# Performance work log

Measured on AMD Instinct MI355X. Metric: run time of the kernel, lower is better.

Reference implementation:

```python
import jax, jax.numpy as jnp
import numpy as np

B = 16
LEN_X = [1024, 896, 768, 640, 512, 1000, 750, 600, 1024, 512, 700, 800, 900, 950, 650, 550]
LEN_M = LEN_X[::-1]
MAXX, MAXM = 1024, 1024
D, H, DH, DFF = 512, 8, 64, 2048
EPS = 1e-5


def _ids(lens):
    seg = np.repeat(np.arange(len(lens)), lens).astype(np.int32)
    pos = np.concatenate([np.arange(l) for l in lens]).astype(np.int32)
    return seg, pos


def _layernorm(x, g, b):
    m = jnp.mean(x, axis=-1, keepdims=True)
    v = jnp.mean((x - m) ** 2, axis=-1, keepdims=True)  # biased var, as torch LN
    return (x - m) * jax.lax.rsqrt(v + EPS) * g + b


def setup_inputs() -> dict:
    key = jax.random.key(0)
    ks = jax.random.split(key, 8)
    TX, TM = sum(LEN_X), sum(LEN_M)
    seg_x, pos_x = _ids(LEN_X)
    seg_m, pos_m = _ids(LEN_M)

    def xavier(k, shape):  # nn.init.xavier_uniform_
        a = float(np.sqrt(6.0 / (shape[0] + shape[1])))
        return jax.random.uniform(k, shape, jnp.float32, -a, a)

    return {
        "x": jax.random.normal(ks[0], (TX, D), jnp.float32),
        "mem": jax.random.normal(ks[1], (TM, D), jnp.float32),
        "Wq": xavier(ks[2], (H * DH, D)),
        "Wk": xavier(ks[3], (H * DH, D)),
        "Wv": xavier(ks[4], (H * DH, D)),
        "Wo": xavier(ks[5], (D, H * DH)),
        "W1": xavier(ks[6], (DFF, D)),
        "b1": jnp.zeros((DFF,), jnp.float32),
        "W2": xavier(ks[7], (D, DFF)),
        "b2": jnp.zeros((D,), jnp.float32),
        "g_in": jnp.ones((D,), jnp.float32),
        "b_in": jnp.zeros((D,), jnp.float32),
        "g_inter": jnp.ones((D,), jnp.float32),
        "b_inter": jnp.zeros((D,), jnp.float32),
        "lengths_x": jnp.array(LEN_X, jnp.int32),
        "lengths_mem": jnp.array(LEN_M, jnp.int32),
        "seg_x": jnp.array(seg_x),
        "pos_x": jnp.array(pos_x),
        "seg_m": jnp.array(seg_m),
        "pos_m": jnp.array(pos_m),
    }


def reference(x, mem, Wq, Wk, Wv, Wo, W1, b1, W2, b2,
              g_in, b_in, g_inter, b_inter,
              lengths_x, lengths_mem, seg_x, pos_x, seg_m, pos_m):
    # --- self_attention(norm_in(x), mem) ---
    h = _layernorm(x, g_in, b_in)
    q = (h @ Wq.T).reshape(-1, H, DH)     # [Tx,H,DH]
    k = (mem @ Wk.T).reshape(-1, H, DH)   # [Tm,H,DH]
    v = (mem @ Wv.T).reshape(-1, H, DH)

    # pad_packed_tensor via scatter (value 0)
    qp = jnp.zeros((B, MAXX, H, DH), q.dtype).at[seg_x, pos_x].set(q)
    kp = jnp.zeros((B, MAXM, H, DH), k.dtype).at[seg_m, pos_m].set(k)
    vp = jnp.zeros((B, MAXM, H, DH), v.dtype).at[seg_m, pos_m].set(v)

    e = jnp.einsum('bxhd,byhd->bhxy', qp, kp) / np.sqrt(DH)  # [B,H,X,Y]

    xm = jnp.arange(MAXX)[None, :] < lengths_x[:, None]   # [B,X]
    ym = jnp.arange(MAXM)[None, :] < lengths_mem[:, None]  # [B,Y]
    mask = (xm[:, :, None] & ym[:, None, :])[:, None]      # [B,1,X,Y]

    e = jnp.where(mask, e, -1e9)
    alpha = jax.nn.softmax(e, axis=-1)
    alpha = jnp.where(mask, alpha, 0.0)

    out = jnp.einsum('bhxy,byhd->bxhd', alpha, vp)         # [B,X,H,DH]
    out = out.reshape(B, MAXX, H * DH) @ Wo.T              # [B,X,D]
    attn = out[seg_x, pos_x]                               # pack_padded_tensor

    x = x + attn
    # --- FFN block ---
    h2 = _layernorm(x, g_inter, b_inter)
    x = x + (jax.nn.relu(h2 @ W1.T + b1) @ W2.T + b2)
    return x
```

## Files before the change

kernel.cpp:

```cpp
#include <hip/hip_runtime.h>

#define TXT 12276
#define DM  512
#define NH  8
#define DHD 64
#define DFF 2048

typedef _Float16 half_t;
typedef _Float16 half8 __attribute__((ext_vector_type(8)));
typedef _Float16 half4v __attribute__((ext_vector_type(4)));
typedef float f32x4 __attribute__((ext_vector_type(4)));

__constant__ int c_offx[16] = {0,1024,1920,2688,3328,3840,4840,5590,6190,7214,7726,8426,9226,10126,11076,11726};
__constant__ int c_lenx[16] = {1024,896,768,640,512,1000,750,600,1024,512,700,800,900,950,650,550};
__constant__ int c_offm[16] = {0,550,1200,2150,3050,3850,4550,5062,6086,6686,7436,8436,8948,9588,10356,11252};
__constant__ int c_lenm[16] = {550,650,950,900,800,700,512,1024,600,750,1000,512,640,768,896,1024};
__constant__ int c_qtcum[17] = {0,16,30,42,52,60,76,88,98,114,122,133,146,161,176,187,196};

enum { EPI_NONE = 0, EPI_RES = 1, EPI_BIAS_RELU = 2, EPI_BIAS_RES = 3 };

__device__ __forceinline__ void gload_lds16(const void* g, void* l) {
    __builtin_amdgcn_global_load_lds((const __attribute__((address_space(1))) uint32_t*)g,
                                     (__attribute__((address_space(3))) uint32_t*)l, 16, 0, 0);
}

template<int EPI, int OUT_HALF, int PIPE>
__global__ __launch_bounds__(256)
void gemm_h(const half_t* __restrict__ A, const half_t* __restrict__ B,
            void* __restrict__ Cv, const float* __restrict__ bias,
            const float* __restrict__ res, int M, int N, int K)
{
    constexpr int NBUF = PIPE ? 2 : 1;
    __shared__ __align__(16) half_t As[NBUF*128*64];
    __shared__ __align__(16) half_t Bs[NBUF*128*64];

    const int t    = threadIdx.x;
    const int lane = t & 63;
    const int wv   = t >> 6;
    const int id   = blockIdx.x;
    const int wid  = (id & 7) * (gridDim.x >> 3) + (id >> 3);
    const int NY   = N >> 7;
    const int m0   = (wid / NY) * 128;
    const int n0   = (wid % NY) * 128;
    const int wr   = (wv >> 1) * 64;
    const int wc   = (wv & 1) * 64;
    const int fr   = lane & 15;
    const int fq   = lane >> 4;
    const int srow   = lane >> 3;
    const int schunk = (lane & 7) ^ srow;

    f32x4 acc[4][4];
    #pragma unroll
    for (int m = 0; m < 4; ++m)
        #pragma unroll
        for (int n = 0; n < 4; ++n) acc[m][n] = (f32x4){0.f,0.f,0.f,0.f};

    auto stage = [&](int k0, half_t* as, half_t* bs) {
        #pragma unroll
        for (int jj = 0; jj < 4; ++jj) {
            const int j    = wv * 4 + jj;
            const int rowt = j * 8 + srow;
            int ra = m0 + rowt; ra = (ra < M) ? ra : (M - 1);
            gload_lds16(A + (size_t)ra * K + k0 + schunk * 8, as + j * 512);
            gload_lds16(B + (size_t)(n0 + rowt) * K + k0 + schunk * 8, bs + j * 512);
        }
    };
    auto compute = [&](const half_t* as, const half_t* bs) {
        #pragma unroll
        for (int kk = 0; kk < 2; ++kk) {
            half8 af[4], bf[4];
            #pragma unroll
            for (int m = 0; m < 4; ++m) {
                const int row  = wr + m * 16 + fr;
                const int boff = (kk * 64 + fq * 16) ^ ((row & 7) << 4);
                af[m] = *(const half8*)((const char*)as + row * 128 + boff);
            }
            #pragma unroll
            for (int n = 0; n < 4; ++n) {
                const int row  = wc + n * 16 + fr;
                const int boff = (kk * 64 + fq * 16) ^ ((row & 7) << 4);
                bf[n] = *(const half8*)((const char*)bs + row * 128 + boff);
            }
            #pragma unroll
            for (int m = 0; m < 4; ++m)
                #pragma unroll
                for (int n = 0; n < 4; ++n)
                    acc[m][n] = __builtin_amdgcn_mfma_f32_16x16x32_f16(af[m], bf[n], acc[m][n], 0, 0, 0);
        }
    };

    if (PIPE == 0) {
        for (int k0 = 0; k0 < K; k0 += 64) {
            stage(k0, As, Bs);
            __syncthreads();
            compute(As, Bs);
            __syncthreads();
        }
    } else {
        stage(0, As, Bs);
        __syncthreads();
        int cur = 0;
        for (int k0 = 0; k0 < K; k0 += 64) {
            if (k0 + 64 < K)
                stage(k0 + 64, As + (cur ^ 1) * 8192, Bs + (cur ^ 1) * 8192);
            compute(As + cur * 8192, Bs + cur * 8192);
            __syncthreads();
            cur ^= 1;
        }
    }

    #pragma unroll
    for (int n = 0; n < 4; ++n) {
        const int col = n0 + wc + n * 16 + fr;
        const float bsv = (EPI == EPI_BIAS_RELU || EPI == EPI_BIAS_RES) ? bias[col] : 0.f;
        #pragma unroll
        for (int m = 0; m < 4; ++m) {
            const f32x4 a = acc[m][n];
            #pragma unroll
            for (int r = 0; r < 4; ++r) {
                const int row = m0 + wr + m * 16 + fq * 4 + r;
                if (row < M) {
                    float v = a[r];
                    if (EPI == EPI_BIAS_RELU || EPI == EPI_BIAS_RES) v += bsv;
                    if (EPI == EPI_BIAS_RELU) v = fmaxf(v, 0.f);
                    if (EPI == EPI_RES || EPI == EPI_BIAS_RES) v += res[(size_t)row * N + col];
                    if (OUT_HALF) ((half_t*)Cv)[(size_t)row * N + col] = (half_t)v;
                    else          ((float*) Cv)[(size_t)row * N + col] = v;
                }
            }
        }
    }
}

__global__ __launch_bounds__(256)
void f2h_w(const float* __restrict__ Wq, const float* __restrict__ Wk,
           const float* __restrict__ Wv, const float* __restrict__ Wo,
           const float* __restrict__ W1, const float* __restrict__ W2,
           half_t* __restrict__ HW)
{
    const int i = blockIdx.x * 256 + threadIdx.x;
    const float* src; int off;
    if      (i < 65536)  { src = Wq; off = 0;      }
    else if (i < 131072) { src = Wk; off = 65536;  }
    else if (i < 196608) { src = Wv; off = 131072; }
    else if (i < 262144) { src = Wo; off = 196608; }
    else if (i < 524288) { src = W1; off = 262144; }
    else                 { src = W2; off = 524288; }
    float4 v = ((const float4*)src)[i - off];
    half4v h = {(_Float16)v.x, (_Float16)v.y, (_Float16)v.z, (_Float16)v.w};
    ((half4v*)HW)[i] = h;
}

__global__ __launch_bounds__(256)
void f2h(const float* __restrict__ in, half_t* __restrict__ out, int n4)
{
    int i = blockIdx.x * 256 + threadIdx.x;
    if (i < n4) {
        float4 v = ((const float4*)in)[i];
        half4v h = {(_Float16)v.x, (_Float16)v.y, (_Float16)v.z, (_Float16)v.w};
        ((half4v*)out)[i] = h;
    }
}

template<int OUT_HALF>
__global__ __launch_bounds__(256)
void layernorm_k(const float* __restrict__ in, const float* __restrict__ g,
                 const float* __restrict__ b, void* __restrict__ outv, int nrows)
{
    const int wave = threadIdx.x >> 6;
    const int lane = threadIdx.x & 63;
    const int row  = blockIdx.x * 4 + wave;
    if (row >= nrows) return;
    const float* px = in + (size_t)row * DM;
    float4 v0 = *(const float4*)(px + lane*4);
    float4 v1 = *(const float4*)(px + 256 + lane*4);

    float s = v0.x+v0.y+v0.z+v0.w + v1.x+v1.y+v1.z+v1.w;
    #pragma unroll
    for (int off = 1; off < 64; off <<= 1) s += __shfl_xor(s, off);
    float mean = s * (1.f/512.f);

    float dx0 = v0.x-mean, dy0 = v0.y-mean, dz0 = v0.z-mean, dw0 = v0.w-mean;
    float dx1 = v1.x-mean, dy1 = v1.y-mean, dz1 = v1.z-mean, dw1 = v1.w-mean;
    float q = dx0*dx0+dy0*dy0+dz0*dz0+dw0*dw0 + dx1*dx1+dy1*dy1+dz1*dz1+dw1*dw1;
    #pragma unroll
    for (int off = 1; off < 64; off <<= 1) q += __shfl_xor(q, off);
    float inv = rsqrtf(q * (1.f/512.f) + 1e-5f);

    float4 g0 = *(const float4*)(g + lane*4);
    float4 g1 = *(const float4*)(g + 256 + lane*4);
    float4 b0 = *(const float4*)(b + lane*4);
    float4 b1 = *(const float4*)(b + 256 + lane*4);
    float4 o0, o1;
    o0.x = dx0*inv*g0.x + b0.x; o0.y = dy0*inv*g0.y + b0.y;
    o0.z = dz0*inv*g0.z + b0.z; o0.w = dw0*inv*g0.w + b0.w;
    o1.x = dx1*inv*g1.x + b1.x; o1.y = dy1*inv*g1.y + b1.y;
    o1.z = dz1*inv*g1.z + b1.z; o1.w = dw1*inv*g1.w + b1.w;

    if (OUT_HALF) {
        half_t* po = (half_t*)outv + (size_t)row * DM;
        half4v h0 = {(_Float16)o0.x,(_Float16)o0.y,(_Float16)o0.z,(_Float16)o0.w};
        half4v h1 = {(_Float16)o1.x,(_Float16)o1.y,(_Float16)o1.z,(_Float16)o1.w};
        *(half4v*)(po + lane*4)       = h0;
        *(half4v*)(po + 256 + lane*4) = h1;
    } else {
        float* po = (float*)outv + (size_t)row * DM;
        *(float4*)(po + lane*4)       = o0;
        *(float4*)(po + 256 + lane*4) = o1;
    }
}

__global__ __launch_bounds__(256)
void attn_k(const half_t* __restrict__ q, const half_t* __restrict__ k,
            const half_t* __restrict__ v, half_t* __restrict__ o, int ldkv)
{
    __shared__ __align__(16) half_t Qs[64*64];
    __shared__ __align__(16) half_t Ks[2][64*64];
    __shared__ __align__(16) half_t Vt[2][64*64];
    __shared__ __align__(16) half_t Ps[4*16*72];

    const int t    = threadIdx.x;
    const int lane = t & 63;
    const int w    = t >> 6;
    const int fr   = lane & 15;
    const int fq   = lane >> 4;
    const int id   = blockIdx.x;
    const int hh   = id & 7;
    const int tile = id >> 3;
    int b = 0;
    while (tile >= c_qtcum[b+1]) ++b;
    const int qt0 = (tile - c_qtcum[b]) * 64;
    const int lx = c_lenx[b], lm = c_lenm[b];
    const int ox = c_offx[b], om = c_offm[b];
    const int qrem = lx - qt0;

    const int srow   = lane >> 3;
    const int schunk = (lane & 7) ^ srow;

    #pragma unroll
    for (int jj = 0; jj < 2; ++jj) {
        const int j   = w * 2 + jj;
        const int row = j * 8 + srow;
        const int rc  = (row < qrem) ? row : qrem - 1;
        gload_lds16(q + (size_t)(ox + qt0 + rc) * DM + hh * DHD + schunk * 8, &Qs[j * 512]);
    }

    const int nt = (lm + 63) >> 6;

    auto stageK = [&](int yt, int buf) {
        const int y0 = yt * 64, yrem = lm - y0;
        #pragma unroll
        for (int jj = 0; jj < 2; ++jj) {
            const int j   = w * 2 + jj;
            const int row = j * 8 + srow;
            const int rc  = (row < yrem) ? row : yrem - 1;
            gload_lds16(k + (size_t)(om + y0 + rc) * ldkv + hh * DHD + schunk * 8, &Ks[buf][j * 512]);
        }
    };
    auto loadV = [&](int yt, half8& va, half8& vb) {
        const int y0 = yt * 64, yrem = lm - y0;
        const int y  = lane;
        const int yc = (y < yrem) ? y : yrem - 1;
        const half_t* vp = v + (size_t)(om + y0 + yc) * ldkv + hh * DHD;
        va = *(const half8*)(vp + w * 8);
        vb = *(const half8*)(vp + (w + 4) * 8);
    };
    auto writeV = [&](int buf, half8 va, half8 vb) {
        const int y = lane;
        #pragma unroll
        for (int jd = 0; jd < 8; ++jd) {
            const int da = w * 8 + jd;
            const int db = (w + 4) * 8 + jd;
            *(half_t*)((char*)&Vt[buf][0] + da * 128 + ((2 * y) ^ ((da & 7) << 4))) = va[jd];
            *(half_t*)((char*)&Vt[buf][0] + db * 128 + ((2 * y) ^ ((db & 7) << 4))) = vb[jd];
        }
    };

    {
        stageK(0, 0);
        half8 va, vb;
        loadV(0, va, vb);
        writeV(0, va, vb);
    }
    __syncthreads();

    f32x4 accO[4];
    float m_run[4], l_run[4];
    #pragma unroll
    for (int r = 0; r < 4; ++r) {
        m_run[r] = -1e30f; l_run[r] = 0.f;
        accO[r] = (f32x4){0.f,0.f,0.f,0.f};
    }

    int buf = 0;
    for (int yt = 0; yt < nt; ++yt) {
        const int yrem = lm - yt * 64;
        const bool pf = (yt + 1 < nt);
        half8 va, vb;
        if (pf) {
            stageK(yt + 1, buf ^ 1);
            loadV(yt + 1, va, vb);
        }

        const half_t* ks = &Ks[buf][0];
        const half_t* vt = &Vt[buf][0];

        f32x4 s[4];
        #pragma unroll
        for (int n = 0; n < 4; ++n) s[n] = (f32x4){0.f,0.f,0.f,0.f};
        #pragma unroll
        for (int kk = 0; kk < 2; ++kk) {
            const int qrow = w * 16 + fr;
            half8 aq = *(const half8*)((const char*)Qs + qrow * 128 + ((kk * 64 + fq * 16) ^ ((qrow & 7) << 4)));
            #pragma unroll
            for (int n = 0; n < 4; ++n) {
                const int krow = n * 16 + fr;
                half8 bk = *(const half8*)((const char*)ks + krow * 128 + ((kk * 64 + fq * 16) ^ ((krow & 7) << 4)));
                s[n] = __builtin_amdgcn_mfma_f32_16x16x32_f16(aq, bk, s[n], 0, 0, 0);
            }
        }

        #pragma unroll
        for (int n = 0; n < 4; ++n) {
            const bool cv = (n * 16 + fr) < yrem;
            #pragma unroll
            for (int r = 0; r < 4; ++r)
                s[n][r] = cv ? s[n][r] * 0.125f : -1e9f;
        }

        #pragma unroll
        for (int r = 0; r < 4; ++r) {
            float mx = fmaxf(fmaxf(s[0][r], s[1][r]), fmaxf(s[2][r], s[3][r]));
            #pragma unroll
            for (int off = 1; off < 16; off <<= 1) mx = fmaxf(mx, __shfl_xor(mx, off));
            const float mnew = fmaxf(m_run[r], mx);
            const float sc   = __expf(m_run[r] - mnew);
            m_run[r] = mnew;
            float rs = 0.f;
            #pragma unroll
            for (int n = 0; n < 4; ++n) {
                const float pv = __expf(s[n][r] - mnew);
                s[n][r] = pv;
                rs += pv;
            }
            #pragma unroll
            for (int off = 1; off < 16; off <<= 1) rs += __shfl_xor(rs, off);
            l_run[r] = l_run[r] * sc + rs;
            #pragma unroll
            for (int n = 0; n < 4; ++n) accO[n][r] *= sc;
        }

        half_t* psw = &Ps[w * 1152];
        #pragma unroll
        for (int n = 0; n < 4; ++n)
            #pragma unroll
            for (int r = 0; r < 4; ++r)
                psw[(fq * 4 + r) * 72 + n * 16 + fr] = (half_t)s[n][r];

        #pragma unroll
        for (int kk = 0; kk < 2; ++kk) {
            half8 ap = *(const half8*)((const char*)psw + fr * 144 + fq * 16 + kk * 64);
            #pragma unroll
            for (int n = 0; n < 4; ++n) {
                const int d = n * 16 + fr;
                half8 bv = *(const half8*)((const char*)vt + d * 128 + ((kk * 64 + fq * 16) ^ ((d & 7) << 4)));
                accO[n] = __builtin_amdgcn_mfma_f32_16x16x32_f16(ap, bv, accO[n], 0, 0, 0);
            }
        }

        if (pf) writeV(buf ^ 1, va, vb);
        __syncthreads();
        buf ^= 1;
    }

    #pragma unroll
    for (int r = 0; r < 4; ++r) {
        const int row = w * 16 + fq * 4 + r;
        if (row < qrem) {
            const float inv = 1.f / l_run[r];
            #pragma unroll
            for (int n = 0; n < 4; ++n)
                o[(size_t)(ox + qt0 + row) * DM + hh * DHD + n * 16 + fr] = (half_t)(accO[n][r] * inv);
        }
    }
}

extern "C" void kernel_launch(void* const* d_in, const int* in_sizes, int n_in,
                              void* d_out, int out_size, void* d_ws, size_t ws_size,
                              hipStream_t stream)
{
    (void)in_sizes; (void)n_in; (void)out_size; (void)ws_size;
    const float* x    = (const float*)d_in[0];
    const float* mem  = (const float*)d_in[1];
    const float* Wq   = (const float*)d_in[2];
    const float* Wk   = (const float*)d_in[3];
    const float* Wv   = (const float*)d_in[4];
    const float* Wo   = (const float*)d_in[5];
    const float* W1   = (const float*)d_in[6];
    const float* b1   = (const float*)d_in[7];
    const float* W2   = (const float*)d_in[8];
    const float* b2   = (const float*)d_in[9];
    const float* g_in = (const float*)d_in[10];
    const float* b_in = (const float*)d_in[11];
    const float* g_it = (const float*)d_in[12];
    const float* b_it = (const float*)d_in[13];
    float* out = (float*)d_out;
    float* ws  = (float*)d_ws;

    const size_t u = (size_t)TXT * DM;
    float*  F0  = ws;
    half_t* H0  = (half_t*)(ws + u);
    half_t* H1  = H0 + u;
    half_t* Hq  = H1 + u;
    half_t* Hkv = Hq + u;
    half_t* HW  = Hkv + 2*u;
    half_t* f1  = H1;

    half_t* hWq = HW;
    half_t* hWk = HW +  262144;
    half_t* hWo = HW +  786432;
    half_t* hW1 = HW + 1048576;
    half_t* hW2 = HW + 2097152;

    const dim3 blk(256);
    const int mt = (TXT + 127) / 128;

    f2h_w<<<dim3(3072), blk, 0, stream>>>(Wq, Wk, Wv, Wo, W1, W2, HW);
    f2h<<<dim3((int)((u/4 + 255) / 256)), blk, 0, stream>>>(mem, H1, (int)(u/4));

    layernorm_k<1><<<dim3(TXT/4), blk, 0, stream>>>(x, g_in, b_in, H0, TXT);

    gemm_h<EPI_NONE,1,1><<<dim3(mt*4), blk, 0, stream>>>(H0, hWq, Hq, nullptr, nullptr, TXT, 512, 512);
    gemm_h<EPI_NONE,1,0><<<dim3(mt*8), blk, 0, stream>>>(H1, hWk, Hkv, nullptr, nullptr, TXT, 1024, 512);

    attn_k<<<dim3(1568), blk, 0, stream>>>(Hq, Hkv, Hkv + 512, H1, 1024);

    gemm_h<EPI_RES,0,1><<<dim3(mt*4), blk, 0, stream>>>(H1, hWo, F0, nullptr, x, TXT, 512, 512);

    layernorm_k<1><<<dim3(TXT/4), blk, 0, stream>>>(F0, g_it, b_it, H0, TXT);

    gemm_h<EPI_BIAS_RELU,1,0><<<dim3(mt*16), blk, 0, stream>>>(H0, hW1, f1, b1, nullptr, TXT, 2048, 512);

    gemm_h<EPI_BIAS_RES,0,1><<<dim3(mt*4), blk, 0, stream>>>(f1, hW2, out, b2, F0, TXT, 512, 2048);
}
```

Baseline: 397.0 us.

## Use vmcnt-based partial waits in GEMM pipeline, transpose attention MFMA layout, fuse conversions

Adds a PIPE=2 GEMM mode that replaces full syncthreads with explicit s_waitcnt vmcnt plus s_barrier, so the next tile's loads can stay in flight while the current tile is computed. The attention kernel swaps the MFMA operand order, which makes each lane own a whole query row, turns the softmax into a scalar running max/sum with two cross-lane shuffles, hoists the Q fragment loads out of the KV loop, and writes the output vectorised. The weight and memory fp32-to-fp16 conversions are merged into one launch. The hand-written vmcnt count assumes a fixed number of outstanding loads per stage, which could cause races if the staging code changes.

```diff
diff --git a/kernel.cpp b/kernel.cpp
--- a/kernel.cpp
+++ b/kernel.cpp
@@ -98,13 +98,27 @@
         }
     } else {
         stage(0, As, Bs);
-        __syncthreads();
+        if (PIPE == 1) __syncthreads();
         int cur = 0;
         for (int k0 = 0; k0 < K; k0 += 64) {
-            if (k0 + 64 < K)
+            const bool nxt = (k0 + 64 < K);
+            if (nxt)
                 stage(k0 + 64, As + (cur ^ 1) * 8192, Bs + (cur ^ 1) * 8192);
+            if (PIPE == 2) {
+                if (nxt) asm volatile("s_waitcnt vmcnt(8)" ::: "memory");
+                else     asm volatile("s_waitcnt vmcnt(0)" ::: "memory");
+                __builtin_amdgcn_s_barrier();
+                asm volatile("" ::: "memory");
+            }
             compute(As + cur * 8192, Bs + cur * 8192);
-            __syncthreads();
+            if (PIPE == 2) {
+                if (nxt) {
+                    asm volatile("" ::: "memory");
+                    __builtin_amdgcn_s_barrier();
+                }
+            } else {
+                __syncthreads();
+            }
             cur ^= 1;
         }
     }
@@ -133,33 +147,24 @@
 }
 
 __global__ __launch_bounds__(256)
-void f2h_w(const float* __restrict__ Wq, const float* __restrict__ Wk,
-           const float* __restrict__ Wv, const float* __restrict__ Wo,
-           const float* __restrict__ W1, const float* __restrict__ W2,
-           half_t* __restrict__ HW)
+void f2h_all(const float* __restrict__ Wq, const float* __restrict__ Wk,
+             const float* __restrict__ Wv, const float* __restrict__ Wo,
+             const float* __restrict__ W1, const float* __restrict__ W2,
+             const float* __restrict__ mem,
+             half_t* __restrict__ HW, half_t* __restrict__ H1)
 {
     const int i = blockIdx.x * 256 + threadIdx.x;
-    const float* src; int off;
-    if      (i < 65536)  { src = Wq; off = 0;      }
-    else if (i < 131072) { src = Wk; off = 65536;  }
-    else if (i < 196608) { src = Wv; off = 131072; }
-    else if (i < 262144) { src = Wo; off = 196608; }
-    else if (i < 524288) { src = W1; off = 262144; }
-    else                 { src = W2; off = 524288; }
+    const float* src; int off; half_t* dst; int dbase;
+    if      (i < 65536)   { src = Wq;  off = 0;       dst = HW; dbase = 0; }
+    else if (i < 131072)  { src = Wk;  off = 65536;   dst = HW; dbase = 0; }
+    else if (i < 196608)  { src = Wv;  off = 131072;  dst = HW; dbase = 0; }
+    else if (i < 262144)  { src = Wo;  off = 196608;  dst = HW; dbase = 0; }
+    else if (i < 524288)  { src = W1;  off = 262144;  dst = HW; dbase = 0; }
+    else if (i < 786432)  { src = W2;  off = 524288;  dst = HW; dbase = 0; }
+    else                  { src = mem; off = 786432;  dst = H1; dbase = 786432; }
     float4 v = ((const float4*)src)[i - off];
     half4v h = {(_Float16)v.x, (_Float16)v.y, (_Float16)v.z, (_Float16)v.w};
-    ((half4v*)HW)[i] = h;
-}
-
-__global__ __launch_bounds__(256)
-void f2h(const float* __restrict__ in, half_t* __restrict__ out, int n4)
-{
-    int i = blockIdx.x * 256 + threadIdx.x;
-    if (i < n4) {
-        float4 v = ((const float4*)in)[i];
-        half4v h = {(_Float16)v.x, (_Float16)v.y, (_Float16)v.z, (_Float16)v.w};
-        ((half4v*)out)[i] = h;
-    }
+    ((half4v*)dst)[i - dbase] = h;
 }
 
 template<int OUT_HALF>
@@ -284,13 +289,14 @@
     }
     __syncthreads();
 
+    const int qrow = w * 16 + fr;
+    const half8 q0 = *(const half8*)((const char*)Qs + qrow * 128 + ((0 * 64 + fq * 16) ^ ((qrow & 7) << 4)));
+    const half8 q1 = *(const half8*)((const char*)Qs + qrow * 128 + ((1 * 64 + fq * 16) ^ ((qrow & 7) << 4)));
+
     f32x4 accO[4];
-    float m_run[4], l_run[4];
-    #pragma unroll
-    for (int r = 0; r < 4; ++r) {
-        m_run[r] = -1e30f; l_run[r] = 0.f;
-        accO[r] = (f32x4){0.f,0.f,0.f,0.f};
-    }
+    float m_run = -1e30f, l_run = 0.f;
+    #pragma unroll
+    for (int n = 0; n < 4; ++n) accO[n] = (f32x4){0.f,0.f,0.f,0.f};
 
     int buf = 0;
     for (int yt = 0; yt < nt; ++yt) {
@@ -310,52 +316,56 @@
         for (int n = 0; n < 4; ++n) s[n] = (f32x4){0.f,0.f,0.f,0.f};
         #pragma unroll
         for (int kk = 0; kk < 2; ++kk) {
-            const int qrow = w * 16 + fr;
-            half8 aq = *(const half8*)((const char*)Qs + qrow * 128 + ((kk * 64 + fq * 16) ^ ((qrow & 7) << 4)));
+            const half8 aq = (kk == 0) ? q0 : q1;
             #pragma unroll
             for (int n = 0; n < 4; ++n) {
                 const int krow = n * 16 + fr;
                 half8 bk = *(const half8*)((const char*)ks + krow * 128 + ((kk * 64 + fq * 16) ^ ((krow & 7) << 4)));
-                s[n] = __builtin_amdgcn_mfma_f32_16x16x32_f16(aq, bk, s[n], 0, 0, 0);
-            }
-        }
-
-        #pragma unroll
-        for (int n = 0; n < 4; ++n) {
-            const bool cv = (n * 16 + fr) < yrem;
-            #pragma unroll
-            for (int r = 0; r < 4; ++r)
-                s[n][r] = cv ? s[n][r] * 0.125f : -1e9f;
-        }
-
-        #pragma unroll
-        for (int r = 0; r < 4; ++r) {
-            float mx = fmaxf(fmaxf(s[0][r], s[1][r]), fmaxf(s[2][r], s[3][r]));
-            #pragma unroll
-            for (int off = 1; off < 16; off <<= 1) mx = fmaxf(mx, __shfl_xor(mx, off));
-            const float mnew = fmaxf(m_run[r], mx);
-            const float sc   = __expf(m_run[r] - mnew);
-            m_run[r] = mnew;
-            float rs = 0.f;
-            #pragma unroll
-            for (int n = 0; n < 4; ++n) {
+                s[n] = __builtin_amdgcn_mfma_f32_16x16x32_f16(bk, aq, s[n], 0, 0, 0);
+            }
+        }
+
+        #pragma unroll
+        for (int n = 0; n < 4; ++n)
+            #pragma unroll
+            for (int r = 0; r < 4; ++r) {
+                const int kv = n * 16 + fq * 4 + r;
+                s[n][r] = (kv < yrem) ? s[n][r] * 0.125f : -1e9f;
+            }
+
+        float mx = s[0][0];
+        #pragma unroll
+        for (int n = 0; n < 4; ++n)
+            #pragma unroll
+            for (int r = 0; r < 4; ++r) mx = fmaxf(mx, s[n][r]);
+        mx = fmaxf(mx, __shfl_xor(mx, 16));
+        mx = fmaxf(mx, __shfl_xor(mx, 32));
+        const float mnew = fmaxf(m_run, mx);
+        const float sc   = __expf(m_run - mnew);
+        m_run = mnew;
+        float rs = 0.f;
+        #pragma unroll
+        for (int n = 0; n < 4; ++n)
+            #pragma unroll
+            for (int r = 0; r < 4; ++r) {
                 const float pv = __expf(s[n][r] - mnew);
                 s[n][r] = pv;
                 rs += pv;
             }
-            #pragma unroll
-            for (int off = 1; off < 16; off <<= 1) rs += __shfl_xor(rs, off);
-            l_run[r] = l_run[r] * sc + rs;
-            #pragma unroll
-            for (int n = 0; n < 4; ++n) accO[n][r] *= sc;
-        }
+        rs += __shfl_xor(rs, 16);
+        rs += __shfl_xor(rs, 32);
+        l_run = l_run * sc + rs;
+        #pragma unroll
+        for (int n = 0; n < 4; ++n)
+            #pragma unroll
+            for (int r = 0; r < 4; ++r) accO[n][r] *= sc;
 
         half_t* psw = &Ps[w * 1152];
         #pragma unroll
         for (int n = 0; n < 4; ++n)
             #pragma unroll
             for (int r = 0; r < 4; ++r)
-                psw[(fq * 4 + r) * 72 + n * 16 + fr] = (half_t)s[n][r];
+                psw[fr * 72 + n * 16 + fq * 4 + r] = (half_t)s[n][r];
 
         #pragma unroll
         for (int kk = 0; kk < 2; ++kk) {
@@ -364,7 +374,7 @@
             for (int n = 0; n < 4; ++n) {
                 const int d = n * 16 + fr;
                 half8 bv = *(const half8*)((const char*)vt + d * 128 + ((kk * 64 + fq * 16) ^ ((d & 7) << 4)));
-                accO[n] = __builtin_amdgcn_mfma_f32_16x16x32_f16(ap, bv, accO[n], 0, 0, 0);
+                accO[n] = __builtin_amdgcn_mfma_f32_16x16x32_f16(bv, ap, accO[n], 0, 0, 0);
             }
         }
 
@@ -373,14 +383,15 @@
         buf ^= 1;
     }
 
-    #pragma unroll
-    for (int r = 0; r < 4; ++r) {
-        const int row = w * 16 + fq * 4 + r;
-        if (row < qrem) {
-            const float inv = 1.f / l_run[r];
-            #pragma unroll
-            for (int n = 0; n < 4; ++n)
-                o[(size_t)(ox + qt0 + row) * DM + hh * DHD + n * 16 + fr] = (half_t)(accO[n][r] * inv);
+    const int qq = w * 16 + fr;
+    if (qq < qrem) {
+        const float inv = 1.f / l_run;
+        half_t* po = o + (size_t)(ox + qt0 + qq) * DM + hh * DHD;
+        #pragma unroll
+        for (int n = 0; n < 4; ++n) {
+            half4v hv = {(_Float16)(accO[n][0] * inv), (_Float16)(accO[n][1] * inv),
+                         (_Float16)(accO[n][2] * inv), (_Float16)(accO[n][3] * inv)};
+            *(half4v*)(po + n * 16 + fq * 4) = hv;
         }
     }
 }
@@ -425,21 +436,20 @@
     const dim3 blk(256);
     const int mt = (TXT + 127) / 128;
 
-    f2h_w<<<dim3(3072), blk, 0, stream>>>(Wq, Wk, Wv, Wo, W1, W2, HW);
-    f2h<<<dim3((int)((u/4 + 255) / 256)), blk, 0, stream>>>(mem, H1, (int)(u/4));
+    f2h_all<<<dim3(9210), blk, 0, stream>>>(Wq, Wk, Wv, Wo, W1, W2, mem, HW, H1);
 
     layernorm_k<1><<<dim3(TXT/4), blk, 0, stream>>>(x, g_in, b_in, H0, TXT);
 
-    gemm_h<EPI_NONE,1,1><<<dim3(mt*4), blk, 0, stream>>>(H0, hWq, Hq, nullptr, nullptr, TXT, 512, 512);
+    gemm_h<EPI_NONE,1,2><<<dim3(mt*4), blk, 0, stream>>>(H0, hWq, Hq, nullptr, nullptr, TXT, 512, 512);
     gemm_h<EPI_NONE,1,0><<<dim3(mt*8), blk, 0, stream>>>(H1, hWk, Hkv, nullptr, nullptr, TXT, 1024, 512);
 
     attn_k<<<dim3(1568), blk, 0, stream>>>(Hq, Hkv, Hkv + 512, H1, 1024);
 
-    gemm_h<EPI_RES,0,1><<<dim3(mt*4), blk, 0, stream>>>(H1, hWo, F0, nullptr, x, TXT, 512, 512);
+    gemm_h<EPI_RES,0,2><<<dim3(mt*4), blk, 0, stream>>>(H1, hWo, F0, nullptr, x, TXT, 512, 512);
 
     layernorm_k<1><<<dim3(TXT/4), blk, 0, stream>>>(F0, g_it, b_it, H0, TXT);
 
     gemm_h<EPI_BIAS_RELU,1,0><<<dim3(mt*16), blk, 0, stream>>>(H0, hW1, f1, b1, nullptr, TXT, 2048, 512);
 
-    gemm_h<EPI_BIAS_RES,0,1><<<dim3(mt*4), blk, 0, stream>>>(f1, hW2, out, b2, F0, TXT, 512, 2048);
-}
+    gemm_h<EPI_BIAS_RES,0,2><<<dim3(mt*4), blk, 0, stream>>>(f1, hW2, out, b2, F0, TXT, 512, 2048);
+}
```

Result: faster. 380.9 us (-4.1%).
